# Kernel optimization log

Measured on AMD Instinct MI355X. Metric: run time of the kernel, lower is better.

Reference implementation:

```python
import jax, jax.numpy as jnp
import numpy as np
from jax import lax

DIM = 96; DSTATE = 16; DCONV = 3; EXPAND = 2
DINNER = DIM * EXPAND            # 192
DTRANK = (DIM + 15) // 16        # 6 = ceil(dim/16)
B = 4; H = 48; W = 48
BN_EPS = 1e-3
LN_EPS = 1e-5


def setup_inputs() -> dict:
    key = jax.random.key(0)
    ks = iter(jax.random.split(key, 32))
    def n(shape, s):
        return jax.random.normal(next(ks), shape, dtype=jnp.float32) * s
    inp = {}
    inp["feature"] = jax.random.normal(next(ks), (B, DIM, H, W), dtype=jnp.float32)
    inp["prediction"] = jax.random.normal(next(ks), (B, 1, H, W), dtype=jnp.float32)
    # norm_pred: BatchNorm2d(1) (eval mode, running stats)
    inp["bnp_g"] = jnp.ones((1,), jnp.float32)
    inp["bnp_b"] = jnp.zeros((1,), jnp.float32)
    inp["bnp_m"] = n((1,), 0.1)
    inp["bnp_v"] = jnp.ones((1,), jnp.float32) + jax.random.uniform(next(ks), (1,)) * 0.1
    # pre_proj: Conv1x1(no bias) + BN + GELU
    inp["pre_w"] = n((DIM, DIM), 0.05)
    inp["pre_bn_g"] = jnp.ones((DIM,), jnp.float32)
    inp["pre_bn_b"] = jnp.zeros((DIM,), jnp.float32)
    inp["pre_bn_m"] = n((DIM,), 0.1)
    inp["pre_bn_v"] = jnp.ones((DIM,), jnp.float32) + jax.random.uniform(next(ks), (DIM,)) * 0.1
    # norm_feature: LayerNorm(dim)
    inp["ln_g"] = jnp.ones((DIM,), jnp.float32)
    inp["ln_b"] = jnp.zeros((DIM,), jnp.float32)
    # SS2D params (VMamba)
    inp["in_proj_w"] = n((2 * DINNER, DIM), 0.05)
    inp["conv_w"] = n((DINNER, 1, DCONV, DCONV), 0.1)   # depthwise
    inp["conv_b"] = jnp.zeros((DINNER,), jnp.float32)
    inp["x_proj_w"] = n((4, DTRANK + 2 * DSTATE, DINNER), 0.05)
    inp["dt_w"] = n((4, DINNER, DTRANK), 0.1)
    inp["dt_b"] = n((4, DINNER), 0.1)
    # S4D-real init: A = -exp(A_logs), A_logs = log(1..N)
    inp["A_logs"] = jnp.log(jnp.tile(jnp.arange(1, DSTATE + 1, dtype=jnp.float32), (4 * DINNER, 1)))
    inp["Ds"] = jnp.ones((4 * DINNER,), jnp.float32)
    inp["onorm_g"] = jnp.ones((DINNER,), jnp.float32)
    inp["onorm_b"] = jnp.zeros((DINNER,), jnp.float32)
    inp["out_proj_w"] = n((DIM, DINNER), 0.05)
    # post_proj: Conv1x1(no bias) + BN + GELU
    inp["post_w"] = n((DIM, DIM), 0.05)
    inp["post_bn_g"] = jnp.ones((DIM,), jnp.float32)
    inp["post_bn_b"] = jnp.zeros((DIM,), jnp.float32)
    inp["post_bn_m"] = n((DIM,), 0.1)
    inp["post_bn_v"] = jnp.ones((DIM,), jnp.float32) + jax.random.uniform(next(ks), (DIM,)) * 0.1
    inp["gate"] = jnp.ones((1,), jnp.float32) * 0.5
    return inp


def _bn(x, g, b, m, v):
    # x: [B,C,H,W]; per-channel eval-mode batchnorm, eps=1e-3
    scale = g / jnp.sqrt(v + BN_EPS)
    return (x - m[None, :, None, None]) * scale[None, :, None, None] + b[None, :, None, None]


def _ln(x, g, b):
    mu = jnp.mean(x, axis=-1, keepdims=True)
    var = jnp.var(x, axis=-1, keepdims=True)
    return (x - mu) / jnp.sqrt(var + LN_EPS) * g + b


def _selective_scan(xs, dts, As, Bs, Cs, Ds, dt_bias):
    # xs,dts: [B,4,D,L]; As: [4,D,N]; Bs,Cs: [B,4,N,L]; Ds,dt_bias: [4,D]
    delta = jax.nn.softplus(dts + dt_bias[None, :, :, None])   # [B,4,D,L]
    u_t = jnp.moveaxis(xs, -1, 0)      # [L,B,4,D]
    d_t = jnp.moveaxis(delta, -1, 0)   # [L,B,4,D]
    B_t = jnp.moveaxis(Bs, -1, 0)      # [L,B,4,N]
    C_t = jnp.moveaxis(Cs, -1, 0)      # [L,B,4,N]
    h0 = jnp.zeros(xs.shape[:3] + (As.shape[-1],), xs.dtype)   # [B,4,D,N]
    def step(h, inp):
        u, d, Bm, Cm = inp
        dA = jnp.exp(d[..., None] * As[None])                     # [B,4,D,N]
        h = h * dA + (d * u)[..., None] * Bm[:, :, None, :]
        y = jnp.einsum('bkdn,bkn->bkd', h, Cm)
        return h, y
    _, ys = lax.scan(step, h0, (u_t, d_t, B_t, C_t))
    y = jnp.moveaxis(ys, 0, -1)        # [B,4,D,L]
    return y + Ds[None, :, :, None] * xs


def _ss2d(x_cl, in_proj_w, conv_w, conv_b, x_proj_w, dt_w, dt_b, A_logs, Ds,
          onorm_g, onorm_b, out_proj_w):
    Bsz, Hh, Ww, _ = x_cl.shape
    di = conv_w.shape[0]
    L = Hh * Ww
    xz = jnp.einsum('bhwc,oc->bhwo', x_cl, in_proj_w)
    x, z = jnp.split(xz, 2, axis=-1)
    xc = jnp.transpose(x, (0, 3, 1, 2))                           # [B,di,H,W]
    pad = (DCONV - 1) // 2
    xc = lax.conv_general_dilated(xc, conv_w, (1, 1), [(pad, pad), (pad, pad)],
                                  dimension_numbers=('NCHW', 'OIHW', 'NCHW'),
                                  feature_group_count=di) + conv_b[None, :, None, None]
    xc = jax.nn.silu(xc)
    # cross-scan: row-major, col-major, and their reverses
    x0 = xc.reshape(Bsz, di, L)
    x1 = jnp.transpose(xc, (0, 1, 3, 2)).reshape(Bsz, di, L)
    xhw = jnp.stack([x0, x1], axis=1)                             # [B,2,di,L]
    xs = jnp.concatenate([xhw, jnp.flip(xhw, axis=-1)], axis=1)   # [B,4,di,L]
    x_dbl = jnp.einsum('bkdl,kcd->bkcl', xs, x_proj_w)
    dts = x_dbl[:, :, :DTRANK]
    Bs = x_dbl[:, :, DTRANK:DTRANK + DSTATE]
    Cs = x_dbl[:, :, DTRANK + DSTATE:]
    dts = jnp.einsum('bkrl,kdr->bkdl', dts, dt_w)
    As = -jnp.exp(A_logs).reshape(4, di, DSTATE)
    out_y = _selective_scan(xs, dts, As, Bs, Cs, Ds.reshape(4, di), dt_b)  # [B,4,di,L]
    inv_y = jnp.flip(out_y[:, 2:4], axis=-1)
    wh = jnp.transpose(out_y[:, 1].reshape(Bsz, di, Ww, Hh), (0, 1, 3, 2)).reshape(Bsz, di, L)
    invwh = jnp.transpose(inv_y[:, 1].reshape(Bsz, di, Ww, Hh), (0, 1, 3, 2)).reshape(Bsz, di, L)
    y = out_y[:, 0] + inv_y[:, 0] + wh + invwh                    # [B,di,L]
    y = jnp.transpose(y.reshape(Bsz, di, Hh, Ww), (0, 2, 3, 1))   # [B,H,W,di]
    y = _ln(y, onorm_g, onorm_b)
    y = y * jax.nn.silu(z)
    return jnp.einsum('bhwd,od->bhwo', y, out_proj_w)


def reference(feature, prediction, bnp_g, bnp_b, bnp_m, bnp_v,
              pre_w, pre_bn_g, pre_bn_b, pre_bn_m, pre_bn_v, ln_g, ln_b,
              in_proj_w, conv_w, conv_b, x_proj_w, dt_w, dt_b, A_logs, Ds,
              onorm_g, onorm_b, out_proj_w,
              post_w, post_bn_g, post_bn_b, post_bn_m, post_bn_v, gate):
    pred_norm = _bn(prediction, bnp_g, bnp_b, bnp_m, bnp_v)
    reverse_mask = 1.0 - jax.nn.sigmoid(pred_norm)
    fm = feature * reverse_mask
    fp = jax.nn.gelu(_bn(jnp.einsum('bchw,oc->bohw', fm, pre_w),
                         pre_bn_g, pre_bn_b, pre_bn_m, pre_bn_v), approximate=False)
    x_cl = _ln(jnp.transpose(fp, (0, 2, 3, 1)), ln_g, ln_b)
    y = _ss2d(x_cl, in_proj_w, conv_w, conv_b, x_proj_w, dt_w, dt_b, A_logs, Ds,
              onorm_g, onorm_b, out_proj_w)
    yr = jnp.transpose(y, (0, 3, 1, 2))
    yr = jax.nn.gelu(_bn(jnp.einsum('bchw,oc->bohw', yr, post_w),
                         post_bn_g, post_bn_b, post_bn_m, post_bn_v), approximate=False)
    return feature + gate[0] * yr
```

## Files before the change

kernel.cpp:

```cpp
#include <hip/hip_runtime.h>
#include <math.h>

#define RFL(x) __builtin_amdgcn_readfirstlane(x)

constexpr int CDIM = 96;
constexpr int DI   = 192;
constexpr int HW   = 48;
constexpr int LL   = 2304;
constexpr int NK   = 4;
constexpr int DST  = 16;
constexpr int DTRK = 6;
constexpr int NCH  = 96;
constexpr int CHK  = 24;
constexpr float LOG2E  = 1.44269504088896f;
constexpr float CBN_EPS = 1e-3f;
constexpr float CLN_EPS = 1e-5f;

__device__ __forceinline__ int Tmap(int x){ return (x % HW) * HW + x / HW; }
__device__ __forceinline__ float siluf(float x){ return x / (1.f + __expf(-x)); }
__device__ __forceinline__ float geluf(float x){ return 0.5f * x * (1.f + erff(x * 0.70710678118654752f)); }
__device__ __forceinline__ int permp(int k, int l){
  if (k == 0) return l;
  if (k == 1) return Tmap(l);
  if (k == 2) return LL - 1 - l;
  return Tmap(LL - 1 - l);
}
__device__ __forceinline__ int lmap(int k, int p){
  if (k == 0) return p;
  if (k == 1) return Tmap(p);
  if (k == 2) return LL - 1 - p;
  return LL - 1 - Tmap(p);
}

__global__ __launch_bounds__(256) void mrr_k0_wcomb(
    const float* __restrict__ post_w, const float* __restrict__ opw,
    const float* __restrict__ conv_w, float* __restrict__ Wc, float* __restrict__ cwT)
{
  int idx = blockIdx.x * 256 + threadIdx.x;
  if (idx < CDIM * DI) {
    int o = idx / DI, d = idx % DI;
    float acc = 0.f;
    for (int c = 0; c < CDIM; ++c)
      acc = fmaf(post_w[o * CDIM + c], opw[c * DI + d], acc);
    Wc[idx] = acc;
  } else if (idx < CDIM * DI + 9 * DI) {
    int t = idx - CDIM * DI;
    int tap = t / DI, d = t % DI;
    cwT[tap * DI + d] = conv_w[d * 9 + tap];
  }
}

__global__ __launch_bounds__(256) void mrr_k1_pre(
    const float* __restrict__ feature, const float* __restrict__ pred,
    const float* __restrict__ bnp_g, const float* __restrict__ bnp_b,
    const float* __restrict__ bnp_m, const float* __restrict__ bnp_v,
    const float* __restrict__ pre_w,
    const float* __restrict__ pbg, const float* __restrict__ pbb,
    const float* __restrict__ pbm, const float* __restrict__ pbv,
    const float* __restrict__ lng, const float* __restrict__ lnb,
    float* __restrict__ x_cl)
{
  __shared__ float s_fm[CDIM][33];
  __shared__ float s_red[16][32];
  __shared__ float s_mu[32], s_rs[32], s_msk[32];
  int tid = threadIdx.x;
  int b = blockIdx.x / 72, p0 = (blockIdx.x % 72) * 32;

  if (tid < 32) {
    float pr = pred[b * LL + p0 + tid];
    float sc = bnp_g[0] * rsqrtf(bnp_v[0] + CBN_EPS);
    float pn = (pr - bnp_m[0]) * sc + bnp_b[0];
    s_msk[tid] = 1.f - 1.f / (1.f + __expf(-pn));
  }
  __syncthreads();
  #pragma unroll
  for (int e = 0; e < 12; ++e) {
    int f = e * 256 + tid;
    int c = f >> 5, px = f & 31;
    s_fm[c][px] = feature[(size_t)(b * CDIM + c) * LL + p0 + px] * s_msk[px];
  }
  __syncthreads();
  int lane = tid & 63;
  int wave = tid >> 6;
  int px = lane & 31, oh = lane >> 5;
  int o0 = wave * 24 + oh * 12;
  float acc[12];
  #pragma unroll
  for (int j = 0; j < 12; ++j) acc[j] = 0.f;
  for (int c = 0; c < CDIM; c += 4) {
    float f0 = s_fm[c][px], f1 = s_fm[c+1][px];
    float f2 = s_fm[c+2][px], f3 = s_fm[c+3][px];
    #pragma unroll
    for (int j = 0; j < 12; ++j) {
      float4 w = *(const float4*)&pre_w[(o0 + j) * CDIM + c];
      acc[j] = fmaf(w.x, f0, fmaf(w.y, f1, fmaf(w.z, f2, fmaf(w.w, f3, acc[j]))));
    }
  }
  float s = 0.f, s2 = 0.f;
  #pragma unroll
  for (int j = 0; j < 12; ++j) {
    int oc = o0 + j;
    float sc = pbg[oc] * rsqrtf(pbv[oc] + CBN_EPS);
    float v = (acc[j] - pbm[oc]) * sc + pbb[oc];
    v = geluf(v);
    acc[j] = v; s += v; s2 = fmaf(v, v, s2);
  }
  int grp = wave * 2 + oh;
  s_red[grp][px] = s; s_red[8 + grp][px] = s2;
  __syncthreads();
  if (tid < 32) {
    float t1 = 0.f, t2 = 0.f;
    #pragma unroll
    for (int q = 0; q < 8; ++q) { t1 += s_red[q][tid]; t2 += s_red[8 + q][tid]; }
    float mu = t1 * (1.f / 96.f);
    float var = t2 * (1.f / 96.f) - mu * mu;
    s_mu[tid] = mu; s_rs[tid] = rsqrtf(var + CLN_EPS);
  }
  __syncthreads();
  float mu = s_mu[px], rs = s_rs[px];
  #pragma unroll
  for (int j = 0; j < 12; ++j) {
    int oc = o0 + j;
    acc[j] = (acc[j] - mu) * rs * lng[oc] + lnb[oc];
  }
  float* dst = &x_cl[(size_t)(b * LL + p0 + px) * CDIM + o0];
  #pragma unroll
  for (int j = 0; j < 12; j += 4)
    *(float4*)(dst + j) = make_float4(acc[j], acc[j+1], acc[j+2], acc[j+3]);
}

__global__ __launch_bounds__(256) void mrr_k2_inproj(
    const float* __restrict__ x_cl, const float* __restrict__ ipw,
    float* __restrict__ xb, float* __restrict__ szb)
{
  __shared__ float s_x[CDIM][65];
  int tid = threadIdx.x;
  int blk = blockIdx.x;
  int b = blk / 144;
  int rem = blk % 144;
  int p0 = (rem % 36) * 64;
  int q = rem / 36;
  #pragma unroll
  for (int e = 0; e < 24; ++e) {
    int f = e * 256 + tid;
    int c = f % CDIM, px = f / CDIM;
    s_x[c][px] = x_cl[(size_t)(b * LL + p0 + px) * CDIM + c];
  }
  __syncthreads();
  int lane = tid & 63;
  int oc0 = RFL(q * 96 + (tid >> 6) * 24);
  float acc[24];
  #pragma unroll
  for (int j = 0; j < 24; ++j) acc[j] = 0.f;
  for (int c = 0; c < CDIM; c += 4) {
    float f0 = s_x[c][lane], f1 = s_x[c+1][lane];
    float f2 = s_x[c+2][lane], f3 = s_x[c+3][lane];
    #pragma unroll
    for (int j = 0; j < 24; ++j) {
      float4 w = *(const float4*)&ipw[(oc0 + j) * CDIM + c];
      acc[j] = fmaf(w.x, f0, fmaf(w.y, f1, fmaf(w.z, f2, fmaf(w.w, f3, acc[j]))));
    }
  }
  int p = p0 + lane;
  if (oc0 < DI) {
    float* dst = &xb[(size_t)(b * LL + p) * DI + oc0];
    #pragma unroll
    for (int j = 0; j < 24; j += 4)
      *(float4*)(dst + j) = make_float4(acc[j], acc[j+1], acc[j+2], acc[j+3]);
  } else {
    #pragma unroll
    for (int j = 0; j < 24; ++j) acc[j] = siluf(acc[j]);
    float* dst = &szb[(size_t)(b * LL + p) * DI + (oc0 - DI)];
    #pragma unroll
    for (int j = 0; j < 24; j += 4)
      *(float4*)(dst + j) = make_float4(acc[j], acc[j+1], acc[j+2], acc[j+3]);
  }
}

__global__ __launch_bounds__(256) void mrr_k3_conv(
    const float* __restrict__ xb, const float* __restrict__ cwT,
    const float* __restrict__ cb, float* __restrict__ xc)
{
  int idx = blockIdx.x * 256 + threadIdx.x;
  int dg = idx % 48;
  int p = (idx / 48) % LL;
  int b = idx / (48 * LL);
  int h = p / HW, w = p % HW;
  float4 acc = ((const float4*)cb)[dg];
  #pragma unroll
  for (int i = 0; i < 3; ++i) {
    int hh = h + i - 1;
    if (hh < 0 || hh >= HW) continue;
    #pragma unroll
    for (int j = 0; j < 3; ++j) {
      int ww = w + j - 1;
      if (ww < 0 || ww >= HW) continue;
      float4 wv = ((const float4*)&cwT[(i * 3 + j) * DI])[dg];
      float4 xv = *(const float4*)&xb[(size_t)(b * LL + hh * HW + ww) * DI + dg * 4];
      acc.x = fmaf(wv.x, xv.x, acc.x);
      acc.y = fmaf(wv.y, xv.y, acc.y);
      acc.z = fmaf(wv.z, xv.z, acc.z);
      acc.w = fmaf(wv.w, xv.w, acc.w);
    }
  }
  acc.x = siluf(acc.x); acc.y = siluf(acc.y); acc.z = siluf(acc.z); acc.w = siluf(acc.w);
  *(float4*)&xc[(size_t)(b * LL + p) * DI + dg * 4] = acc;
}

__global__ __launch_bounds__(640) void mrr_k4_proj(
    const float* __restrict__ xc, const float* __restrict__ xpw,
    const float* __restrict__ dtw, const float* __restrict__ dtb,
    float* __restrict__ delta, float* __restrict__ Bsb, float* __restrict__ Csb)
{
  __shared__ float s_u[DI][72];
  __shared__ float s_w[48][164];
  __shared__ float s_dtr[NK][DTRK][64];
  __shared__ float s_dtwf[NK * DI * DTRK];
  __shared__ float s_dtbf[NK * DI];
  int tid = threadIdx.x;
  int b = blockIdx.x / 36, p0 = (blockIdx.x % 36) * 64;
  int b4 = b * NK;

  for (int f = tid; f < DI * 64; f += 640) {
    int d_ = f % DI, px = f / DI;
    s_u[d_][px] = xc[(size_t)(b * LL + p0 + px) * DI + d_];
  }
  for (int f = tid; f < NK * DI * DTRK; f += 640) s_dtwf[f] = dtw[f];
  for (int f = tid; f < NK * DI; f += 640) s_dtbf[f] = dtb[f];

  int rg = tid >> 4;
  int pg = tid & 15;
  float acc[4][4];
  #pragma unroll
  for (int i = 0; i < 4; ++i)
    #pragma unroll
    for (int j = 0; j < 4; ++j) acc[i][j] = 0.f;

  for (int ch = 0; ch < 4; ++ch) {
    int c0 = ch * 48;
    if (ch) __syncthreads();
    for (int f = tid; f < 152 * 48; f += 640) {
      int cl = f % 48, row = f / 48;
      int kk = row / 38, rr = row % 38;
      s_w[cl][kk * 40 + rr] = xpw[row * DI + c0 + cl];
    }
    __syncthreads();
    #pragma unroll 4
    for (int cc = 0; cc < 48; ++cc) {
      float4 wv = *(const float4*)&s_w[cc][rg << 2];
      float4 uv = *(const float4*)&s_u[c0 + cc][pg << 2];
      acc[0][0] = fmaf(wv.x, uv.x, acc[0][0]); acc[0][1] = fmaf(wv.x, uv.y, acc[0][1]);
      acc[0][2] = fmaf(wv.x, uv.z, acc[0][2]); acc[0][3] = fmaf(wv.x, uv.w, acc[0][3]);
      acc[1][0] = fmaf(wv.y, uv.x, acc[1][0]); acc[1][1] = fmaf(wv.y, uv.y, acc[1][1]);
      acc[1][2] = fmaf(wv.y, uv.z, acc[1][2]); acc[1][3] = fmaf(wv.y, uv.w, acc[1][3]);
      acc[2][0] = fmaf(wv.z, uv.x, acc[2][0]); acc[2][1] = fmaf(wv.z, uv.y, acc[2][1]);
      acc[2][2] = fmaf(wv.z, uv.z, acc[2][2]); acc[2][3] = fmaf(wv.z, uv.w, acc[2][3]);
      acc[3][0] = fmaf(wv.w, uv.x, acc[3][0]); acc[3][1] = fmaf(wv.w, uv.y, acc[3][1]);
      acc[3][2] = fmaf(wv.w, uv.z, acc[3][2]); acc[3][3] = fmaf(wv.w, uv.w, acc[3][3]);
    }
  }

  #pragma unroll
  for (int i = 0; i < 4; ++i) {
    int rp = (rg << 2) + i;
    int kk = rp / 40, rr = rp % 40;
    if (rr < DTRK) {
      #pragma unroll
      for (int j = 0; j < 4; ++j) s_dtr[kk][rr][(pg << 2) + j] = acc[i][j];
    } else if (rr < DTRK + DST) {
      int n = rr - DTRK;
      #pragma unroll
      for (int j = 0; j < 4; ++j) {
        int l = lmap(kk, p0 + (pg << 2) + j);
        Bsb[(size_t)((b4 + kk) * LL + l) * DST + n] = acc[i][j];
      }
    } else if (rr < DTRK + 2 * DST) {
      int n = rr - DTRK - DST;
      #pragma unroll
      for (int j = 0; j < 4; ++j) {
        int l = lmap(kk, p0 + (pg << 2) + j);
        Csb[(size_t)((b4 + kk) * LL + l) * DST + n] = acc[i][j];
      }
    }
  }
  __syncthreads();

  int lane = tid & 63;
  int wv_ = tid >> 6;
  for (int unit = wv_; unit < 64; unit += 10) {
    int kk = unit >> 4, pxq = unit & 15;
    float dtr[6][4];
    #pragma unroll
    for (int rr = 0; rr < 6; ++rr)
      #pragma unroll
      for (int j = 0; j < 4; ++j)
        dtr[rr][j] = s_dtr[kk][rr][(pxq << 2) + j];
    #pragma unroll
    for (int dch = 0; dch < 3; ++dch) {
      int d_ = dch * 64 + lane;
      int kdl = kk * DI + d_;
      float w0 = s_dtwf[kdl * 6 + 0], w1 = s_dtwf[kdl * 6 + 1], w2 = s_dtwf[kdl * 6 + 2];
      float w3 = s_dtwf[kdl * 6 + 3], w4 = s_dtwf[kdl * 6 + 4], w5 = s_dtwf[kdl * 6 + 5];
      float bias = s_dtbf[kdl];
      #pragma unroll
      for (int j = 0; j < 4; ++j) {
        float sv = bias;
        sv = fmaf(w0, dtr[0][j], sv); sv = fmaf(w1, dtr[1][j], sv);
        sv = fmaf(w2, dtr[2][j], sv); sv = fmaf(w3, dtr[3][j], sv);
        sv = fmaf(w4, dtr[4][j], sv); sv = fmaf(w5, dtr[5][j], sv);
        float sp = fmaxf(sv, 0.f) + __logf(1.f + __expf(-fabsf(sv)));
        int l = lmap(kk, p0 + (pxq << 2) + j);
        delta[(size_t)((b4 + kk) * LL + l) * DI + d_] = sp;
      }
    }
  }
}

#define SSTEP(n, Bc, Cc, yy) { float dA = exp2f(A2[n] * dv); hh[n] = fmaf(hh[n], dA, du * (Bc)); yy = fmaf(hh[n], (Cc), yy); }

__global__ __launch_bounds__(256) void mrr_k5_scan1(
    const float* __restrict__ xc,
    const float* __restrict__ Bsb, const float* __restrict__ Csb,
    const float* __restrict__ A_logs,
    float* __restrict__ delta,
    float* __restrict__ yb, float* __restrict__ hend, float* __restrict__ Ssum)
{
  int lane = threadIdx.x & 63;
  int wid = RFL(blockIdx.x * 4 + (threadIdx.x >> 6));
  int c = wid % NCH;
  int r = wid / NCH;
  int dch = r % 3;
  int k = (r / 3) % NK;
  int b = r / (3 * NK);
  int d = dch * 64 + lane;
  int kd = k * DI + d;

  float A2[16];
  {
    const float4* Ap = (const float4*)&A_logs[(size_t)kd * 16];
    #pragma unroll
    for (int i = 0; i < 4; ++i) {
      float4 a = Ap[i];
      A2[4*i+0] = -exp2f(a.x * LOG2E) * LOG2E;
      A2[4*i+1] = -exp2f(a.y * LOG2E) * LOG2E;
      A2[4*i+2] = -exp2f(a.z * LOG2E) * LOG2E;
      A2[4*i+3] = -exp2f(a.w * LOG2E) * LOG2E;
    }
  }
  float hh[16];
  #pragma unroll
  for (int n = 0; n < 16; ++n) hh[n] = 0.f;
  float S = 0.f;
  int l0 = c * CHK;
  int bk = b * NK + k;
  size_t ebase = (size_t)(bk * LL + l0) * DI + d;
  size_t bbase = (size_t)(bk * LL + l0) * DST;
  float dv = delta[ebase];
  float u  = xc[(size_t)(b * LL + permp(k, l0)) * DI + d];
  const float4* Bp = (const float4*)(Bsb + bbase);
  const float4* Cp = (const float4*)(Csb + bbase);
  float4 B0 = Bp[0], B1 = Bp[1], B2 = Bp[2], B3 = Bp[3];
  float4 C0 = Cp[0], C1 = Cp[1], C2 = Cp[2], C3 = Cp[3];
  for (int t = 0; t < CHK; ++t) {
    int tn = (t < CHK - 1) ? t + 1 : t;
    float ndv = delta[ebase + (size_t)tn * DI];
    float nu  = xc[(size_t)(b * LL + permp(k, l0 + tn)) * DI + d];
    const float4* nBp = (const float4*)(Bsb + bbase + (size_t)tn * DST);
    const float4* nCp = (const float4*)(Csb + bbase + (size_t)tn * DST);
    float4 nB0 = nBp[0], nB1 = nBp[1], nB2 = nBp[2], nB3 = nBp[3];
    float4 nC0 = nCp[0], nC1 = nCp[1], nC2 = nCp[2], nC3 = nCp[3];
    float du = dv * u;
    float y0 = 0.f, y1 = 0.f, y2 = 0.f, y3 = 0.f;
    SSTEP(0,  B0.x, C0.x, y0) SSTEP(1,  B0.y, C0.y, y1) SSTEP(2,  B0.z, C0.z, y2) SSTEP(3,  B0.w, C0.w, y3)
    SSTEP(4,  B1.x, C1.x, y0) SSTEP(5,  B1.y, C1.y, y1) SSTEP(6,  B1.z, C1.z, y2) SSTEP(7,  B1.w, C1.w, y3)
    SSTEP(8,  B2.x, C2.x, y0) SSTEP(9,  B2.y, C2.y, y1) SSTEP(10, B2.z, C2.z, y2) SSTEP(11, B2.w, C2.w, y3)
    SSTEP(12, B3.x, C3.x, y0) SSTEP(13, B3.y, C3.y, y1) SSTEP(14, B3.z, C3.z, y2) SSTEP(15, B3.w, C3.w, y3)
    yb[ebase + (size_t)t * DI] = (y0 + y1) + (y2 + y3);
    S += dv;
    delta[ebase + (size_t)t * DI] = S;
    dv = ndv; u = nu;
    B0 = nB0; B1 = nB1; B2 = nB2; B3 = nB3;
    C0 = nC0; C1 = nC1; C2 = nC2; C3 = nC3;
  }
  int gg = bk * 3 + dch;
  size_t hb = ((size_t)(gg * NCH + c) * 64 + lane) * 16;
  float4* Hp = (float4*)&hend[hb];
  Hp[0] = make_float4(hh[0], hh[1], hh[2], hh[3]);
  Hp[1] = make_float4(hh[4], hh[5], hh[6], hh[7]);
  Hp[2] = make_float4(hh[8], hh[9], hh[10], hh[11]);
  Hp[3] = make_float4(hh[12], hh[13], hh[14], hh[15]);
  Ssum[(size_t)(gg * NCH + c) * 64 + lane] = S;
}

__global__ __launch_bounds__(1024) void mrr_k5_mid(
    float* __restrict__ hend, const float* __restrict__ Ssum,
    const float* __restrict__ A_logs)
{
  int t = blockIdx.x * 1024 + threadIdx.x;
  int n = t & 15;
  int g = t >> 4;
  int ln = g & 63;
  int gg = g >> 6;
  int dch = gg % 3;
  int k = (gg / 3) % NK;
  int d = dch * 64 + ln;
  float AL = A_logs[(size_t)(k * DI + d) * 16 + n];
  float A2 = -exp2f(AL * LOG2E) * LOG2E;
  float hi = 0.f;
  for (int c = 0; c < NCH; ++c) {
    size_t a = ((size_t)(gg * NCH + c) * 64 + ln) * 16 + n;
    float tmp = hend[a];
    float S = Ssum[(size_t)(gg * NCH + c) * 64 + ln];
    hend[a] = hi;
    hi = tmp + exp2f(A2 * S) * hi;
  }
}

#define CSTEP(n, Cc, yy) { float e = exp2f(A2[n] * cum); yy = fmaf(e * gi[n], (Cc), yy); }

__global__ __launch_bounds__(256) void mrr_k5_scan2(
    const float* __restrict__ cumd, const float* __restrict__ Csb,
    const float* __restrict__ A_logs, const float* __restrict__ hinit,
    float* __restrict__ yb)
{
  int lane = threadIdx.x & 63;
  int wid = RFL(blockIdx.x * 4 + (threadIdx.x >> 6));
  int c = wid % NCH;
  if (c == 0) return;
  int r = wid / NCH;
  int dch = r % 3;
  int k = (r / 3) % NK;
  int b = r / (3 * NK);
  int d = dch * 64 + lane;
  int kd = k * DI + d;
  float A2[16];
  {
    const float4* Ap = (const float4*)&A_logs[(size_t)kd * 16];
    #pragma unroll
    for (int i = 0; i < 4; ++i) {
      float4 a = Ap[i];
      A2[4*i+0] = -exp2f(a.x * LOG2E) * LOG2E;
      A2[4*i+1] = -exp2f(a.y * LOG2E) * LOG2E;
      A2[4*i+2] = -exp2f(a.z * LOG2E) * LOG2E;
      A2[4*i+3] = -exp2f(a.w * LOG2E) * LOG2E;
    }
  }
  int bk = b * NK + k;
  int gg = bk * 3 + dch;
  float gi[16];
  {
    const float4* Gp = (const float4*)&hinit[((size_t)(gg * NCH + c) * 64 + lane) * 16];
    float4 g0 = Gp[0], g1 = Gp[1], g2 = Gp[2], g3 = Gp[3];
    gi[0]=g0.x; gi[1]=g0.y; gi[2]=g0.z; gi[3]=g0.w;
    gi[4]=g1.x; gi[5]=g1.y; gi[6]=g1.z; gi[7]=g1.w;
    gi[8]=g2.x; gi[9]=g2.y; gi[10]=g2.z; gi[11]=g2.w;
    gi[12]=g3.x; gi[13]=g3.y; gi[14]=g3.z; gi[15]=g3.w;
  }
  int l0 = c * CHK;
  size_t ebase = (size_t)(bk * LL + l0) * DI + d;
  size_t bbase = (size_t)(bk * LL + l0) * DST;
  #pragma unroll 2
  for (int t = 0; t < CHK; ++t) {
    float cum = cumd[ebase + (size_t)t * DI];
    const float4* Cp = (const float4*)(Csb + bbase + (size_t)t * DST);
    float4 C0 = Cp[0], C1 = Cp[1], C2 = Cp[2], C3 = Cp[3];
    float y0 = 0.f, y1 = 0.f, y2 = 0.f, y3 = 0.f;
    CSTEP(0,  C0.x, y0) CSTEP(1,  C0.y, y1) CSTEP(2,  C0.z, y2) CSTEP(3,  C0.w, y3)
    CSTEP(4,  C1.x, y0) CSTEP(5,  C1.y, y1) CSTEP(6,  C1.z, y2) CSTEP(7,  C1.w, y3)
    CSTEP(8,  C2.x, y0) CSTEP(9,  C2.y, y1) CSTEP(10, C2.z, y2) CSTEP(11, C2.w, y3)
    CSTEP(12, C3.x, y0) CSTEP(13, C3.y, y1) CSTEP(14, C3.z, y2) CSTEP(15, C3.w, y3)
    yb[ebase + (size_t)t * DI] += (y0 + y1) + (y2 + y3);
  }
}

__global__ __launch_bounds__(512) void mrr_k6_out(
    const float* __restrict__ yb, const float* __restrict__ xc,
    const float* __restrict__ szb, const float* __restrict__ Ds,
    const float* __restrict__ ong, const float* __restrict__ onb,
    const float* __restrict__ Wc,
    const float* __restrict__ qbg, const float* __restrict__ qbb,
    const float* __restrict__ qbm, const float* __restrict__ qbv,
    const float* __restrict__ feature, const float* __restrict__ gate,
    float* __restrict__ out)
{
  __shared__ float s_t[DI][33];
  __shared__ float s_red[32][32];
  __shared__ float s_mu[32], s_rs[32];
  int tid = threadIdx.x;
  int b = blockIdx.x / 72, p0 = (blockIdx.x % 72) * 32;
  int b4 = b * NK;
  #pragma unroll
  for (int e = 0; e < 12; ++e) {
    int f = e * 512 + tid;
    int d = f % DI, px = f / DI;
    int p = p0 + px;
    int tp = Tmap(p);
    float t0 = yb[(size_t)((b4 + 0) * LL + p) * DI + d];
    float t1 = yb[(size_t)((b4 + 1) * LL + tp) * DI + d];
    float t2 = yb[(size_t)((b4 + 2) * LL + (LL - 1 - p)) * DI + d];
    float t3 = yb[(size_t)((b4 + 3) * LL + (LL - 1 - tp)) * DI + d];
    float Dv = Ds[d] + Ds[DI + d] + Ds[2 * DI + d] + Ds[3 * DI + d];
    float tv = t0 + t1 + t2 + t3 + Dv * xc[(size_t)(b * LL + p) * DI + d];
    s_t[d][px] = tv;
  }
  __syncthreads();
  {
    int q = tid >> 5, px = tid & 31;
    float s = 0.f, s2 = 0.f;
    #pragma unroll
    for (int i = 0; i < 12; ++i) {
      float v = s_t[q * 12 + i][px];
      s += v; s2 = fmaf(v, v, s2);
    }
    s_red[q][px] = s; s_red[16 + q][px] = s2;
  }
  __syncthreads();
  if (tid < 32) {
    float s = 0.f, s2 = 0.f;
    #pragma unroll
    for (int q = 0; q < 16; ++q) { s += s_red[q][tid]; s2 += s_red[16 + q][tid]; }
    float mu = s * (1.f / (float)DI);
    float var = s2 * (1.f / (float)DI) - mu * mu;
    s_mu[tid] = mu; s_rs[tid] = rsqrtf(var + CLN_EPS);
  }
  __syncthreads();
  #pragma unroll
  for (int e = 0; e < 12; ++e) {
    int f = e * 512 + tid;
    int d = f % DI, px = f / DI;
    int p = p0 + px;
    float v = s_t[d][px];
    v = (v - s_mu[px]) * s_rs[px] * ong[d] + onb[d];
    v *= szb[(size_t)(b * LL + p) * DI + d];
    s_t[d][px] = v;
  }
  __syncthreads();
  int lane = tid & 63;
  int wave = tid >> 6;
  int px = lane & 31, oh = lane >> 5;
  int o0 = wave * 12 + oh * 6;
  float acc[6] = {0.f, 0.f, 0.f, 0.f, 0.f, 0.f};
  for (int dd = 0; dd < DI; dd += 4) {
    float f0 = s_t[dd][px], f1 = s_t[dd+1][px];
    float f2 = s_t[dd+2][px], f3 = s_t[dd+3][px];
    #pragma unroll
    for (int j = 0; j < 6; ++j) {
      float4 w = *(const float4*)&Wc[(o0 + j) * DI + dd];
      acc[j] = fmaf(w.x, f0, fmaf(w.y, f1, fmaf(w.z, f2, fmaf(w.w, f3, acc[j]))));
    }
  }
  float gt = gate[0];
  #pragma unroll
  for (int j = 0; j < 6; ++j) {
    int o = o0 + j;
    float sc = qbg[o] * rsqrtf(qbv[o] + CBN_EPS);
    float v = (acc[j] - qbm[o]) * sc + qbb[o];
    v = geluf(v);
    size_t oi = (size_t)(b * CDIM + o) * LL + p0 + px;
    out[oi] = feature[oi] + gt * v;
  }
}

extern "C" void kernel_launch(void* const* d_in, const int* in_sizes, int n_in,
                              void* d_out, int out_size, void* d_ws, size_t ws_size,
                              hipStream_t stream)
{
  (void)in_sizes; (void)n_in; (void)out_size; (void)ws_size;
  const float* feature    = (const float*)d_in[0];
  const float* prediction = (const float*)d_in[1];
  const float* bnp_g      = (const float*)d_in[2];
  const float* bnp_b      = (const float*)d_in[3];
  const float* bnp_m      = (const float*)d_in[4];
  const float* bnp_v      = (const float*)d_in[5];
  const float* pre_w      = (const float*)d_in[6];
  const float* pre_bn_g   = (const float*)d_in[7];
  const float* pre_bn_b   = (const float*)d_in[8];
  const float* pre_bn_m   = (const float*)d_in[9];
  const float* pre_bn_v   = (const float*)d_in[10];
  const float* ln_g       = (const float*)d_in[11];
  const float* ln_b       = (const float*)d_in[12];
  const float* in_proj_w  = (const float*)d_in[13];
  const float* conv_w     = (const float*)d_in[14];
  const float* conv_b     = (const float*)d_in[15];
  const float* x_proj_w   = (const float*)d_in[16];
  const float* dt_w       = (const float*)d_in[17];
  const float* dt_b       = (const float*)d_in[18];
  const float* A_logs     = (const float*)d_in[19];
  const float* Ds         = (const float*)d_in[20];
  const float* onorm_g    = (const float*)d_in[21];
  const float* onorm_b    = (const float*)d_in[22];
  const float* out_proj_w = (const float*)d_in[23];
  const float* post_w     = (const float*)d_in[24];
  const float* post_bn_g  = (const float*)d_in[25];
  const float* post_bn_b  = (const float*)d_in[26];
  const float* post_bn_m  = (const float*)d_in[27];
  const float* post_bn_v  = (const float*)d_in[28];
  const float* gate       = (const float*)d_in[29];
  float* out = (float*)d_out;

  float* ws    = (float*)d_ws;
  float* Wc    = ws;
  float* x_cl  = Wc    + 18432;
  float* xb    = x_cl  + 884736;
  float* szb   = xb    + 1769472;
  float* xcb   = szb   + 1769472;
  float* dlt   = xcb   + 1769472;
  float* Bsb   = dlt   + 7077888;
  float* Csb   = Bsb   + 589824;
  float* yb    = Csb   + 589824;
  float* hend  = yb    + 7077888;
  float* Ss    = hend  + 4718592;
  float* cwT   = Ss    + 294912;

  mrr_k0_wcomb<<<dim3(79), dim3(256), 0, stream>>>(post_w, out_proj_w, conv_w, Wc, cwT);
  mrr_k1_pre<<<dim3(288), dim3(256), 0, stream>>>(feature, prediction,
      bnp_g, bnp_b, bnp_m, bnp_v, pre_w,
      pre_bn_g, pre_bn_b, pre_bn_m, pre_bn_v, ln_g, ln_b, x_cl);
  mrr_k2_inproj<<<dim3(576), dim3(256), 0, stream>>>(x_cl, in_proj_w, xb, szb);
  mrr_k3_conv<<<dim3(1728), dim3(256), 0, stream>>>(xb, cwT, conv_b, xcb);
  mrr_k4_proj<<<dim3(144), dim3(640), 0, stream>>>(xcb, x_proj_w, dt_w, dt_b, dlt, Bsb, Csb);
  mrr_k5_scan1<<<dim3(1152), dim3(256), 0, stream>>>(xcb, Bsb, Csb, A_logs, dlt, yb, hend, Ss);
  mrr_k5_mid<<<dim3(48), dim3(1024), 0, stream>>>(hend, Ss, A_logs);
  mrr_k5_scan2<<<dim3(1152), dim3(256), 0, stream>>>(dlt, Csb, A_logs, hend, yb);
  mrr_k6_out<<<dim3(288), dim3(512), 0, stream>>>(yb, xcb, szb, Ds, onorm_g, onorm_b,
      Wc, post_bn_g, post_bn_b, post_bn_m, post_bn_v, feature, gate, out);
}
```

Measured before the change: 383.7 us.

## Retile pre/in-proj/x-proj kernels and prefetch in carry-propagation scan

The pre-projection and in-projection kernels move to 1024-thread blocks covering 64 pixels, with fewer output channels per thread. The x-projection kernel shrinks to 16-pixel tiles with 320 threads and more blocks, and reads the dt weights directly from global memory instead of staging them in shared memory. The mid scan kernel uses smaller blocks (more blocks) and prefetches the next chunk's state and sum one iteration ahead. The aim is better occupancy, more parallelism across CUs and hidden load latency, at the cost of reloading the x_proj weights into shared memory in many more blocks and lower per-thread register reuse.

New measurement: 382.9 us. Within noise of the previous version (-0.2%).

```diff
diff --git a/kernel.cpp b/kernel.cpp
--- a/kernel.cpp
+++ b/kernel.cpp
@@ -50,7 +50,7 @@
   }
 }
 
-__global__ __launch_bounds__(256) void mrr_k1_pre(
+__global__ __launch_bounds__(1024) void mrr_k1_pre(
     const float* __restrict__ feature, const float* __restrict__ pred,
     const float* __restrict__ bnp_g, const float* __restrict__ bnp_b,
     const float* __restrict__ bnp_m, const float* __restrict__ bnp_v,
@@ -60,13 +60,14 @@
     const float* __restrict__ lng, const float* __restrict__ lnb,
     float* __restrict__ x_cl)
 {
-  __shared__ float s_fm[CDIM][33];
-  __shared__ float s_red[16][32];
-  __shared__ float s_mu[32], s_rs[32], s_msk[32];
+  __shared__ float s_fm[CDIM][65];
+  __shared__ float s_red1[16][64];
+  __shared__ float s_red2[16][64];
+  __shared__ float s_mu[64], s_rs[64], s_msk[64];
   int tid = threadIdx.x;
-  int b = blockIdx.x / 72, p0 = (blockIdx.x % 72) * 32;
-
-  if (tid < 32) {
+  int b = blockIdx.x / 36, p0 = (blockIdx.x % 36) * 64;
+
+  if (tid < 64) {
     float pr = pred[b * LL + p0 + tid];
     float sc = bnp_g[0] * rsqrtf(bnp_v[0] + CBN_EPS);
     float pn = (pr - bnp_m[0]) * sc + bnp_b[0];
@@ -74,105 +75,101 @@
   }
   __syncthreads();
   #pragma unroll
-  for (int e = 0; e < 12; ++e) {
-    int f = e * 256 + tid;
-    int c = f >> 5, px = f & 31;
+  for (int e = 0; e < 6; ++e) {
+    int f = e * 1024 + tid;
+    int c = f >> 6, px = f & 63;
     s_fm[c][px] = feature[(size_t)(b * CDIM + c) * LL + p0 + px] * s_msk[px];
   }
   __syncthreads();
   int lane = tid & 63;
   int wave = tid >> 6;
-  int px = lane & 31, oh = lane >> 5;
-  int o0 = wave * 24 + oh * 12;
-  float acc[12];
-  #pragma unroll
-  for (int j = 0; j < 12; ++j) acc[j] = 0.f;
+  int o0 = RFL(wave * 6);
+  float acc[6] = {0.f, 0.f, 0.f, 0.f, 0.f, 0.f};
   for (int c = 0; c < CDIM; c += 4) {
-    float f0 = s_fm[c][px], f1 = s_fm[c+1][px];
-    float f2 = s_fm[c+2][px], f3 = s_fm[c+3][px];
-    #pragma unroll
-    for (int j = 0; j < 12; ++j) {
+    float f0 = s_fm[c][lane], f1 = s_fm[c+1][lane];
+    float f2 = s_fm[c+2][lane], f3 = s_fm[c+3][lane];
+    #pragma unroll
+    for (int j = 0; j < 6; ++j) {
       float4 w = *(const float4*)&pre_w[(o0 + j) * CDIM + c];
       acc[j] = fmaf(w.x, f0, fmaf(w.y, f1, fmaf(w.z, f2, fmaf(w.w, f3, acc[j]))));
     }
   }
   float s = 0.f, s2 = 0.f;
   #pragma unroll
-  for (int j = 0; j < 12; ++j) {
+  for (int j = 0; j < 6; ++j) {
     int oc = o0 + j;
     float sc = pbg[oc] * rsqrtf(pbv[oc] + CBN_EPS);
     float v = (acc[j] - pbm[oc]) * sc + pbb[oc];
     v = geluf(v);
     acc[j] = v; s += v; s2 = fmaf(v, v, s2);
   }
-  int grp = wave * 2 + oh;
-  s_red[grp][px] = s; s_red[8 + grp][px] = s2;
-  __syncthreads();
-  if (tid < 32) {
+  s_red1[wave][lane] = s; s_red2[wave][lane] = s2;
+  __syncthreads();
+  if (tid < 64) {
     float t1 = 0.f, t2 = 0.f;
     #pragma unroll
-    for (int q = 0; q < 8; ++q) { t1 += s_red[q][tid]; t2 += s_red[8 + q][tid]; }
+    for (int q = 0; q < 16; ++q) { t1 += s_red1[q][tid]; t2 += s_red2[q][tid]; }
     float mu = t1 * (1.f / 96.f);
     float var = t2 * (1.f / 96.f) - mu * mu;
     s_mu[tid] = mu; s_rs[tid] = rsqrtf(var + CLN_EPS);
   }
   __syncthreads();
-  float mu = s_mu[px], rs = s_rs[px];
-  #pragma unroll
-  for (int j = 0; j < 12; ++j) {
+  float mu = s_mu[lane], rs = s_rs[lane];
+  #pragma unroll
+  for (int j = 0; j < 6; ++j) {
     int oc = o0 + j;
     acc[j] = (acc[j] - mu) * rs * lng[oc] + lnb[oc];
   }
-  float* dst = &x_cl[(size_t)(b * LL + p0 + px) * CDIM + o0];
-  #pragma unroll
-  for (int j = 0; j < 12; j += 4)
-    *(float4*)(dst + j) = make_float4(acc[j], acc[j+1], acc[j+2], acc[j+3]);
-}
-
-__global__ __launch_bounds__(256) void mrr_k2_inproj(
+  float* dst = &x_cl[(size_t)(b * LL + p0 + lane) * CDIM + o0];
+  #pragma unroll
+  for (int j = 0; j < 6; j += 2)
+    *(float2*)(dst + j) = make_float2(acc[j], acc[j+1]);
+}
+
+__global__ __launch_bounds__(1024) void mrr_k2_inproj(
     const float* __restrict__ x_cl, const float* __restrict__ ipw,
     float* __restrict__ xb, float* __restrict__ szb)
 {
   __shared__ float s_x[CDIM][65];
   int tid = threadIdx.x;
   int blk = blockIdx.x;
-  int b = blk / 144;
-  int rem = blk % 144;
+  int b = blk / 72;
+  int rem = blk % 72;
   int p0 = (rem % 36) * 64;
-  int q = rem / 36;
-  #pragma unroll
-  for (int e = 0; e < 24; ++e) {
-    int f = e * 256 + tid;
+  int half = rem / 36;
+  #pragma unroll
+  for (int e = 0; e < 6; ++e) {
+    int f = e * 1024 + tid;
     int c = f % CDIM, px = f / CDIM;
     s_x[c][px] = x_cl[(size_t)(b * LL + p0 + px) * CDIM + c];
   }
   __syncthreads();
   int lane = tid & 63;
-  int oc0 = RFL(q * 96 + (tid >> 6) * 24);
-  float acc[24];
-  #pragma unroll
-  for (int j = 0; j < 24; ++j) acc[j] = 0.f;
+  int oc0 = RFL(half * 192 + (tid >> 6) * 12);
+  float acc[12];
+  #pragma unroll
+  for (int j = 0; j < 12; ++j) acc[j] = 0.f;
   for (int c = 0; c < CDIM; c += 4) {
     float f0 = s_x[c][lane], f1 = s_x[c+1][lane];
     float f2 = s_x[c+2][lane], f3 = s_x[c+3][lane];
     #pragma unroll
-    for (int j = 0; j < 24; ++j) {
+    for (int j = 0; j < 12; ++j) {
       float4 w = *(const float4*)&ipw[(oc0 + j) * CDIM + c];
       acc[j] = fmaf(w.x, f0, fmaf(w.y, f1, fmaf(w.z, f2, fmaf(w.w, f3, acc[j]))));
     }
   }
   int p = p0 + lane;
-  if (oc0 < DI) {
+  if (half == 0) {
     float* dst = &xb[(size_t)(b * LL + p) * DI + oc0];
     #pragma unroll
-    for (int j = 0; j < 24; j += 4)
+    for (int j = 0; j < 12; j += 4)
       *(float4*)(dst + j) = make_float4(acc[j], acc[j+1], acc[j+2], acc[j+3]);
   } else {
     #pragma unroll
-    for (int j = 0; j < 24; ++j) acc[j] = siluf(acc[j]);
+    for (int j = 0; j < 12; ++j) acc[j] = siluf(acc[j]);
     float* dst = &szb[(size_t)(b * LL + p) * DI + (oc0 - DI)];
     #pragma unroll
-    for (int j = 0; j < 24; j += 4)
+    for (int j = 0; j < 12; j += 4)
       *(float4*)(dst + j) = make_float4(acc[j], acc[j+1], acc[j+2], acc[j+3]);
   }
 }
@@ -207,39 +204,35 @@
   *(float4*)&xc[(size_t)(b * LL + p) * DI + dg * 4] = acc;
 }
 
-__global__ __launch_bounds__(640) void mrr_k4_proj(
+__global__ __launch_bounds__(320) void mrr_k4_proj(
     const float* __restrict__ xc, const float* __restrict__ xpw,
     const float* __restrict__ dtw, const float* __restrict__ dtb,
     float* __restrict__ delta, float* __restrict__ Bsb, float* __restrict__ Csb)
 {
-  __shared__ float s_u[DI][72];
+  __shared__ float s_u[DI][20];
   __shared__ float s_w[48][164];
-  __shared__ float s_dtr[NK][DTRK][64];
-  __shared__ float s_dtwf[NK * DI * DTRK];
-  __shared__ float s_dtbf[NK * DI];
+  __shared__ float s_dtr[NK][DTRK][16];
   int tid = threadIdx.x;
-  int b = blockIdx.x / 36, p0 = (blockIdx.x % 36) * 64;
+  int b = blockIdx.x / 144, p0 = (blockIdx.x % 144) * 16;
   int b4 = b * NK;
 
-  for (int f = tid; f < DI * 64; f += 640) {
+  for (int f = tid; f < DI * 16; f += 320) {
     int d_ = f % DI, px = f / DI;
     s_u[d_][px] = xc[(size_t)(b * LL + p0 + px) * DI + d_];
   }
-  for (int f = tid; f < NK * DI * DTRK; f += 640) s_dtwf[f] = dtw[f];
-  for (int f = tid; f < NK * DI; f += 640) s_dtbf[f] = dtb[f];
-
-  int rg = tid >> 4;
-  int pg = tid & 15;
-  float acc[4][4];
-  #pragma unroll
-  for (int i = 0; i < 4; ++i)
+
+  int rg = tid >> 2;
+  int pg = tid & 3;
+  float acc[2][4];
+  #pragma unroll
+  for (int i = 0; i < 2; ++i)
     #pragma unroll
     for (int j = 0; j < 4; ++j) acc[i][j] = 0.f;
 
   for (int ch = 0; ch < 4; ++ch) {
     int c0 = ch * 48;
     if (ch) __syncthreads();
-    for (int f = tid; f < 152 * 48; f += 640) {
+    for (int f = tid; f < 152 * 48; f += 320) {
       int cl = f % 48, row = f / 48;
       int kk = row / 38, rr = row % 38;
       s_w[cl][kk * 40 + rr] = xpw[row * DI + c0 + cl];
@@ -247,22 +240,18 @@
     __syncthreads();
     #pragma unroll 4
     for (int cc = 0; cc < 48; ++cc) {
-      float4 wv = *(const float4*)&s_w[cc][rg << 2];
+      float2 wv = *(const float2*)&s_w[cc][rg << 1];
       float4 uv = *(const float4*)&s_u[c0 + cc][pg << 2];
       acc[0][0] = fmaf(wv.x, uv.x, acc[0][0]); acc[0][1] = fmaf(wv.x, uv.y, acc[0][1]);
       acc[0][2] = fmaf(wv.x, uv.z, acc[0][2]); acc[0][3] = fmaf(wv.x, uv.w, acc[0][3]);
       acc[1][0] = fmaf(wv.y, uv.x, acc[1][0]); acc[1][1] = fmaf(wv.y, uv.y, acc[1][1]);
       acc[1][2] = fmaf(wv.y, uv.z, acc[1][2]); acc[1][3] = fmaf(wv.y, uv.w, acc[1][3]);
-      acc[2][0] = fmaf(wv.z, uv.x, acc[2][0]); acc[2][1] = fmaf(wv.z, uv.y, acc[2][1]);
-      acc[2][2] = fmaf(wv.z, uv.z, acc[2][2]); acc[2][3] = fmaf(wv.z, uv.w, acc[2][3]);
-      acc[3][0] = fmaf(wv.w, uv.x, acc[3][0]); acc[3][1] = fmaf(wv.w, uv.y, acc[3][1]);
-      acc[3][2] = fmaf(wv.w, uv.z, acc[3][2]); acc[3][3] = fmaf(wv.w, uv.w, acc[3][3]);
-    }
-  }
-
-  #pragma unroll
-  for (int i = 0; i < 4; ++i) {
-    int rp = (rg << 2) + i;
+    }
+  }
+
+  #pragma unroll
+  for (int i = 0; i < 2; ++i) {
+    int rp = (rg << 1) + i;
     int kk = rp / 40, rr = rp % 40;
     if (rr < DTRK) {
       #pragma unroll
@@ -287,8 +276,8 @@
 
   int lane = tid & 63;
   int wv_ = tid >> 6;
-  for (int unit = wv_; unit < 64; unit += 10) {
-    int kk = unit >> 4, pxq = unit & 15;
+  for (int unit = wv_; unit < 16; unit += 5) {
+    int kk = unit >> 2, pxq = unit & 3;
     float dtr[6][4];
     #pragma unroll
     for (int rr = 0; rr < 6; ++rr)
@@ -299,9 +288,9 @@
     for (int dch = 0; dch < 3; ++dch) {
       int d_ = dch * 64 + lane;
       int kdl = kk * DI + d_;
-      float w0 = s_dtwf[kdl * 6 + 0], w1 = s_dtwf[kdl * 6 + 1], w2 = s_dtwf[kdl * 6 + 2];
-      float w3 = s_dtwf[kdl * 6 + 3], w4 = s_dtwf[kdl * 6 + 4], w5 = s_dtwf[kdl * 6 + 5];
-      float bias = s_dtbf[kdl];
+      float w0 = dtw[kdl * 6 + 0], w1 = dtw[kdl * 6 + 1], w2 = dtw[kdl * 6 + 2];
+      float w3 = dtw[kdl * 6 + 3], w4 = dtw[kdl * 6 + 4], w5 = dtw[kdl * 6 + 5];
+      float bias = dtb[kdl];
       #pragma unroll
       for (int j = 0; j < 4; ++j) {
         float sv = bias;
@@ -392,11 +381,11 @@
   Ssum[(size_t)(gg * NCH + c) * 64 + lane] = S;
 }
 
-__global__ __launch_bounds__(1024) void mrr_k5_mid(
+__global__ __launch_bounds__(512) void mrr_k5_mid(
     float* __restrict__ hend, const float* __restrict__ Ssum,
     const float* __restrict__ A_logs)
 {
-  int t = blockIdx.x * 1024 + threadIdx.x;
+  int t = blockIdx.x * 512 + threadIdx.x;
   int n = t & 15;
   int g = t >> 4;
   int ln = g & 63;
@@ -407,12 +396,18 @@
   float AL = A_logs[(size_t)(k * DI + d) * 16 + n];
   float A2 = -exp2f(AL * LOG2E) * LOG2E;
   float hi = 0.f;
+  size_t base = ((size_t)(gg * NCH) * 64 + ln) * 16 + n;
+  size_t sbase = (size_t)(gg * NCH) * 64 + ln;
+  float nh = hend[base];
+  float nS = Ssum[sbase];
   for (int c = 0; c < NCH; ++c) {
-    size_t a = ((size_t)(gg * NCH + c) * 64 + ln) * 16 + n;
-    float tmp = hend[a];
-    float S = Ssum[(size_t)(gg * NCH + c) * 64 + ln];
-    hend[a] = hi;
-    hi = tmp + exp2f(A2 * S) * hi;
+    float hc = nh, Sc = nS;
+    if (c + 1 < NCH) {
+      nh = hend[base + (size_t)(c + 1) * 1024];
+      nS = Ssum[sbase + (size_t)(c + 1) * 64];
+    }
+    hend[base + (size_t)c * 1024] = hi;
+    hi = hc + exp2f(A2 * Sc) * hi;
   }
 }
 
@@ -613,14 +608,14 @@
   float* cwT   = Ss    + 294912;
 
   mrr_k0_wcomb<<<dim3(79), dim3(256), 0, stream>>>(post_w, out_proj_w, conv_w, Wc, cwT);
-  mrr_k1_pre<<<dim3(288), dim3(256), 0, stream>>>(feature, prediction,
+  mrr_k1_pre<<<dim3(144), dim3(1024), 0, stream>>>(feature, prediction,
       bnp_g, bnp_b, bnp_m, bnp_v, pre_w,
       pre_bn_g, pre_bn_b, pre_bn_m, pre_bn_v, ln_g, ln_b, x_cl);
-  mrr_k2_inproj<<<dim3(576), dim3(256), 0, stream>>>(x_cl, in_proj_w, xb, szb);
+  mrr_k2_inproj<<<dim3(288), dim3(1024), 0, stream>>>(x_cl, in_proj_w, xb, szb);
   mrr_k3_conv<<<dim3(1728), dim3(256), 0, stream>>>(xb, cwT, conv_b, xcb);
-  mrr_k4_proj<<<dim3(144), dim3(640), 0, stream>>>(xcb, x_proj_w, dt_w, dt_b, dlt, Bsb, Csb);
+  mrr_k4_proj<<<dim3(576), dim3(320), 0, stream>>>(xcb, x_proj_w, dt_w, dt_b, dlt, Bsb, Csb);
   mrr_k5_scan1<<<dim3(1152), dim3(256), 0, stream>>>(xcb, Bsb, Csb, A_logs, dlt, yb, hend, Ss);
-  mrr_k5_mid<<<dim3(48), dim3(1024), 0, stream>>>(hend, Ss, A_logs);
+  mrr_k5_mid<<<dim3(96), dim3(512), 0, stream>>>(hend, Ss, A_logs);
   mrr_k5_scan2<<<dim3(1152), dim3(256), 0, stream>>>(dlt, Csb, A_logs, hend, yb);
   mrr_k6_out<<<dim3(288), dim3(512), 0, stream>>>(yb, xcb, szb, Ds, onorm_g, onorm_b,
       Wc, post_bn_g, post_bn_b, post_bn_m, post_bn_v, feature, gate, out);
```
